# Kernel optimization log

Measured on AMD Instinct MI355X. Metric: run time of the kernel, lower is better.

The kernel has to match this reference:

```python
import jax, jax.numpy as jnp
import numpy as np

B, E, H = 16384, 1024, 16
LN_EPS = 1e-5


def setup_inputs() -> dict:
    key = jax.random.key(0)
    ks = jax.random.split(key, 16)
    s = 0.02  # xavier-ish init scale
    inp = {
        "id_feat": jax.random.normal(ks[0], (B, E), jnp.float32),
        "txt_feat": jax.random.normal(ks[1], (B, E), jnp.float32),
        "vis_feat": jax.random.normal(ks[2], (B, E), jnp.float32),
    }
    i = 3
    for name in ("id", "txt", "vis"):
        inp[f"w_in_{name}"] = jax.random.normal(ks[i], (3 * E, E), jnp.float32) * s; i += 1
        inp[f"b_in_{name}"] = jnp.zeros((3 * E,), jnp.float32)
        inp[f"w_out_{name}"] = jax.random.normal(ks[i], (E, E), jnp.float32) * s; i += 1
        inp[f"b_out_{name}"] = jnp.zeros((E,), jnp.float32)
    inp["w_fuse"] = jax.random.normal(ks[i], (E, 3 * E), jnp.float32) * s
    inp["b_fuse"] = jnp.zeros((E,), jnp.float32)
    inp["ln_g"] = jnp.ones((E,), jnp.float32)
    inp["ln_b"] = jnp.zeros((E,), jnp.float32)
    return inp


def _mha(q, kv, w_in, b_in, w_out, b_out):
    """torch nn.MultiheadAttention (batch_first, eval mode). q: [B,1,E], kv: [B,K,E]."""
    D = E // H
    wq, wk, wv = jnp.split(w_in, 3, axis=0)
    bq, bk, bv = jnp.split(b_in, 3)
    K = kv.shape[1]
    qh = (q @ wq.T + bq).reshape(-1, 1, H, D).transpose(0, 2, 1, 3)   # [B,H,1,D]
    kh = (kv @ wk.T + bk).reshape(-1, K, H, D).transpose(0, 2, 1, 3)  # [B,H,K,D]
    vh = (kv @ wv.T + bv).reshape(-1, K, H, D).transpose(0, 2, 1, 3)
    scores = jnp.einsum('bhqd,bhkd->bhqk', qh, kh) / jnp.sqrt(jnp.float32(D))
    attn = jax.nn.softmax(scores, axis=-1)
    o = jnp.einsum('bhqk,bhkd->bhqd', attn, vh).transpose(0, 2, 1, 3).reshape(-1, E)
    return o @ w_out.T + b_out  # [B,E]


def reference(id_feat, txt_feat, vis_feat,
              w_in_id, b_in_id, w_out_id, b_out_id,
              w_in_txt, b_in_txt, w_out_txt, b_out_txt,
              w_in_vis, b_in_vis, w_out_vis, b_out_vis,
              w_fuse, b_fuse, ln_g, ln_b):
    idq, txtq, visq = id_feat[:, None], txt_feat[:, None], vis_feat[:, None]
    a_id = _mha(idq, jnp.concatenate([txtq, visq], axis=1), w_in_id, b_in_id, w_out_id, b_out_id)
    a_txt = _mha(txtq, jnp.concatenate([idq, visq], axis=1), w_in_txt, b_in_txt, w_out_txt, b_out_txt)
    a_vis = _mha(visq, jnp.concatenate([idq, txtq], axis=1), w_in_vis, b_in_vis, w_out_vis, b_out_vis)
    concat = jnp.concatenate([a_id, a_txt, a_vis], axis=1)  # [B, 3E]
    y = concat @ w_fuse.T + b_fuse
    mu = jnp.mean(y, axis=-1, keepdims=True)
    var = jnp.var(y, axis=-1, keepdims=True)
    return (y - mu) / jnp.sqrt(var + LN_EPS) * ln_g + ln_b
```

## Files before the change

kernel.cpp:

```cpp
#include <hip/hip_runtime.h>
#include <stdint.h>

#define B_ROWS 16384
#define E_DIM 1024
#define H_N 16

typedef unsigned short u16;
typedef __attribute__((ext_vector_type(4))) float f32x4;
typedef __attribute__((ext_vector_type(4))) unsigned short u16x4;
typedef __attribute__((ext_vector_type(8))) short bf16x8;

static __device__ __forceinline__ u16 f2bf(float f) {
  union { float f; unsigned u; } x; x.f = f;
  unsigned r = (x.u + 0x7FFFu + ((x.u >> 16) & 1u)) >> 16;
  return (u16)r;
}
static __device__ __forceinline__ float bf2f(u16 h) {
  union { unsigned u; float f; } x; x.u = ((unsigned)h) << 16;
  return x.f;
}

typedef const __attribute__((address_space(1))) void gvoid;
typedef __attribute__((address_space(3))) void lvoid;
static __device__ __forceinline__ void gload16(const void* g, void* l) {
  __builtin_amdgcn_global_load_lds((gvoid*)g, (lvoid*)l, 16, 0, 0);
}

__global__ __launch_bounds__(256) void cvt_f32_bf16(const float* __restrict__ in,
                                                    u16* __restrict__ out, int n4) {
  int stride = gridDim.x * blockDim.x;
  for (int i = blockIdx.x * blockDim.x + threadIdx.x; i < n4; i += stride) {
    f32x4 v = ((const f32x4*)in)[i];
    u16x4 o;
    o.x = f2bf(v.x); o.y = f2bf(v.y); o.z = f2bf(v.z); o.w = f2bf(v.w);
    ((u16x4*)out)[i] = o;
  }
}

__global__ __launch_bounds__(256) void cvt3_f32_bf16(const float* __restrict__ i0,
                                                     const float* __restrict__ i1,
                                                     const float* __restrict__ i2,
                                                     u16* __restrict__ o0,
                                                     u16* __restrict__ o1,
                                                     u16* __restrict__ o2, int n4) {
  int stride = gridDim.x * blockDim.x;
  for (int i = blockIdx.x * blockDim.x + threadIdx.x; i < n4; i += stride) {
    f32x4 a = ((const f32x4*)i0)[i];
    f32x4 b = ((const f32x4*)i1)[i];
    f32x4 c = ((const f32x4*)i2)[i];
    u16x4 x, y, z;
    x.x = f2bf(a.x); x.y = f2bf(a.y); x.z = f2bf(a.z); x.w = f2bf(a.w);
    y.x = f2bf(b.x); y.y = f2bf(b.y); y.z = f2bf(b.z); y.w = f2bf(b.w);
    z.x = f2bf(c.x); z.y = f2bf(c.y); z.z = f2bf(c.z); z.w = f2bf(c.w);
    ((u16x4*)o0)[i] = x;
    ((u16x4*)o1)[i] = y;
    ((u16x4*)o2)[i] = z;
  }
}

__global__ __launch_bounds__(256) void transpose_to_bf16(const float* __restrict__ in,
                                                         u16* __restrict__ out, int n) {
  __shared__ float t[32][33];
  int bx = blockIdx.x * 32;
  int by = blockIdx.y * 32;
  int tx = threadIdx.x, ty = threadIdx.y;
  for (int r = ty; r < 32; r += 8)
    t[r][tx] = in[(size_t)(by + r) * n + bx + tx];
  __syncthreads();
  for (int r = ty; r < 32; r += 8)
    out[(size_t)(bx + r) * n + by + tx] = f2bf(t[tx][r]);
}

__global__ __launch_bounds__(256) void fold_bias(const float* __restrict__ b0,
                                                 const float* __restrict__ b1,
                                                 const float* __restrict__ b2,
                                                 const float* __restrict__ wfuse,
                                                 const float* __restrict__ bfuse,
                                                 float* __restrict__ cb) {
  int wave = threadIdx.x >> 6, lane = threadIdx.x & 63;
  int j = blockIdx.x * 4 + wave;
  const float* wrow = wfuse + (size_t)j * (3 * E_DIM);
  float s = 0.f;
  for (int i = lane; i < E_DIM; i += 64) s += b0[i] * wrow[i];
  for (int i = lane; i < E_DIM; i += 64) s += b1[i] * wrow[E_DIM + i];
  for (int i = lane; i < E_DIM; i += 64) s += b2[i] * wrow[2 * E_DIM + i];
  for (int off = 32; off; off >>= 1) s += __shfl_xor(s, off);
  if (lane == 0) cb[j] = bfuse[j] + s;
}

__global__ __launch_bounds__(256) void concat_bias(const float* __restrict__ bq,
                                                   const float* __restrict__ bo0,
                                                   const float* __restrict__ bo1,
                                                   float* __restrict__ out) {
  int i = blockIdx.x * 256 + threadIdx.x;
  float v;
  if (i < 1024) v = bq[i];
  else if (i < 3072) v = bo0[i];
  else v = bo1[i - 2048];
  out[i] = v;
}

#define BM 256
#define BN 256
#define BK 64

#define RDA(buf, qm, dst)                                                         \
  do {                                                                            \
    _Pragma("unroll") for (int m = 0; m < 4; m++)                                 \
    _Pragma("unroll") for (int kk = 0; kk < 2; kk++) {                            \
      int rl = (qm)*64 + m * 16 + l16;                                            \
      int col = ((kk * 64 + kq * 16) ^ ((l16 & 7) << 4)) >> 1;                    \
      dst[m][kk] = *(const bf16x8*)&lds[buf][wm * 8192 + rl * 64 + col];          \
    }                                                                             \
  } while (0)

#define RDB(buf, qn, dst)                                                         \
  do {                                                                            \
    _Pragma("unroll") for (int n = 0; n < 2; n++)                                 \
    _Pragma("unroll") for (int kk = 0; kk < 2; kk++) {                            \
      int rt = (qn)*128 + wn * 32 + n * 16 + l16;           \
      int col = ((kk * 64 + kq * 16) ^ ((l16 & 7) << 4)) >> 1;                    \
      dst[n][kk] = *(const bf16x8*)&lds[buf][16384 + (rt >> 7) * 8192 +           \
                                             (rt & 127) * 64 + col];              \
    }                                                                             \
  } while (0)

#define MMAQ(qm, qn, A_, B_)                                                      \
  do {                                                                            \
    __builtin_amdgcn_s_setprio(1);                                                \
    _Pragma("unroll") for (int m = 0; m < 4; m++)                                 \
    _Pragma("unroll") for (int n = 0; n < 2; n++)                                 \
    _Pragma("unroll") for (int kk = 0; kk < 2; kk++)                              \
      acc[(qm)*4 + m][(qn)*2 + n] = __builtin_amdgcn_mfma_f32_16x16x32_bf16(      \
          A_[m][kk], B_[n][kk], acc[(qm)*4 + m][(qn)*2 + n], 0, 0, 0);            \
    __builtin_amdgcn_s_setprio(0);                                                \
  } while (0)

#define BAR() __builtin_amdgcn_s_barrier()
#define SCHED() __builtin_amdgcn_sched_barrier(0)
#define LGKM0() asm volatile("s_waitcnt lgkmcnt(0)" ::: "memory")
#define VMC(n) asm volatile("s_waitcnt vmcnt(" #n ")" ::: "memory")

template <int MODE>
__global__ __launch_bounds__(512, 2) void gemm256(const u16* __restrict__ A,
                                                  const u16* __restrict__ W,
                                                  void* __restrict__ Cp,
                                                  const float* __restrict__ bias,
                                                  int lda, int ldw, int ldc, int K,
                                                  int nbn, int njb,
                                                  long jsA, long jsW, long jsC, long jsB) {
  __shared__ __align__(16) u16 lds[2][32768];

  const int tid = threadIdx.x;
  const int wave = tid >> 6;
  const int lane = tid & 63;
  const int wm = wave >> 2;
  const int wn = wave & 3;
  const int l16 = lane & 15;
  const int kq = lane >> 4;

  const int nwg = gridDim.x;
  int bid = blockIdx.x;
  int xcd = bid & 7, orig = bid >> 3;
  int q8 = nwg >> 3, r8 = nwg & 7;
  int wg = (xcd < r8 ? xcd * (q8 + 1) : r8 * (q8 + 1) + (xcd - r8) * q8) + orig;
  const int j = wg / njb;
  const int rem = wg - j * njb;
  const int bm = rem / nbn;
  const int bn = rem % nbn;

  const u16* Ab = A + j * jsA + (size_t)bm * BM * lda;
  const u16* Wb = W + j * jsW + (size_t)bn * BN * ldw;

  f32x4 acc[8][4];
#pragma unroll
  for (int i = 0; i < 8; i++)
#pragma unroll
    for (int n = 0; n < 4; n++) acc[i][n] = (f32x4){0.f, 0.f, 0.f, 0.f};

  auto stageH = [&](int buf, int which, int k0) {
    const u16* src = (which >= 2) ? Wb : Ab;
    const int ld = (which >= 2) ? ldw : lda;
    const int h = which & 1;
#pragma unroll
    for (int r = 0; r < 2; r++) {
      int slot = r * 512 + tid;
      int row = h * 128 + (slot >> 3);
      int col = ((slot & 7) ^ (row & 7)) * 8;
      gload16(src + (size_t)row * ld + k0 + col, &lds[buf][which * 8192 + slot * 8]);
    }
  };

  const int nt = K / BK;
  stageH(0, 0, 0); stageH(0, 1, 0); stageH(0, 2, 0); stageH(0, 3, 0);
  VMC(2);
  BAR();
  SCHED();

  bf16x8 a[4][2], b0[2][2], b1[2][2];
  int cur = 0;
  for (int t = 0; t < nt; ++t) {
    const bool pf = (t + 1 < nt);
    const int nb = cur ^ 1;
    const int nk = (t + 1) * BK;
    RDA(cur, 0, a);
    RDB(cur, 0, b0);
    if (pf) { stageH(nb, 0, nk); stageH(nb, 1, nk); stageH(nb, 2, nk); }
    BAR();
    LGKM0();
    SCHED();
    MMAQ(0, 0, a, b0);
    if (pf) VMC(6); else VMC(0);
    BAR();
    SCHED();
    RDB(cur, 1, b1);
    if (pf) stageH(nb, 3, nk);
    BAR();
    LGKM0();
    SCHED();
    MMAQ(0, 1, a, b1);
    BAR();
    RDA(cur, 1, a);
    BAR();
    LGKM0();
    SCHED();
    MMAQ(1, 0, a, b0);
    BAR();
    MMAQ(1, 1, a, b1);
    if (pf) VMC(2); else VMC(0);
    BAR();
    SCHED();
    cur ^= 1;
  }

  const int r0 = kq * 4;
#pragma unroll
  for (int mf = 0; mf < 8; mf++) {
#pragma unroll
    for (int nf = 0; nf < 4; nf++) {
      int row = bm * BM + wm * 128 + mf * 16 + r0;
      int col = bn * BN + (nf >> 1) * 128 + wn * 32 + (nf & 1) * 16 + l16;
      if (MODE == 0) {
        u16* C = (u16*)Cp + j * jsC;
        float bv = bias ? bias[j * jsB + col] : 0.f;
#pragma unroll
        for (int r = 0; r < 4; r++)
          C[(size_t)(row + r) * ldc + col] = f2bf(acc[mf][nf][r] + bv);
      } else {
        float* C = (float*)Cp + j * jsC;
        float bv = bias[j * jsB + col];
#pragma unroll
        for (int r = 0; r < 4; r++)
          C[(size_t)(row + r) * ldc + col] = acc[mf][nf][r] + bv;
      }
    }
  }
}

__global__ __launch_bounds__(256) void attn_combine3(const u16* __restrict__ Pb,
                                                     long jsP, u16* __restrict__ Oc) {
  int gw = blockIdx.x * 4 + (threadIdx.x >> 6);
  int lane = threadIdx.x & 63;
  int b = gw >> 4, h = gw & 15;
  int d = h * 64 + lane;
  size_t prow = (size_t)b * 5120;
  const int j1a[3] = {1, 0, 0}, j2a[3] = {2, 2, 1};
  const int offA[3] = {1024, 1024, 3072}, offB[3] = {1024, 3072, 3072};
#pragma unroll
  for (int m = 0; m < 3; m++) {
    const u16* Pq = Pb + m * jsP;
    const u16* Pa = Pb + j1a[m] * jsP;
    const u16* Pc = Pb + j2a[m] * jsP;
    float q = bf2f(Pq[prow + d]);
    float k1 = bf2f(Pa[prow + offA[m] + d]);
    float v1 = bf2f(Pa[prow + offA[m] + 1024 + d]);
    float k2 = bf2f(Pc[prow + offB[m] + d]);
    float v2 = bf2f(Pc[prow + offB[m] + 1024 + d]);
    float s1 = q * k1, s2 = q * k2;
    for (int off = 32; off; off >>= 1) {
      s1 += __shfl_xor(s1, off);
      s2 += __shfl_xor(s2, off);
    }
    s1 *= 0.125f; s2 *= 0.125f;
    float mx = fmaxf(s1, s2);
    float e1 = __expf(s1 - mx), e2 = __expf(s2 - mx);
    float rn = 1.f / (e1 + e2);
    Oc[(size_t)b * 3072 + m * 1024 + d] = f2bf((e1 * rn) * v1 + (e2 * rn) * v2);
  }
}

__global__ __launch_bounds__(256) void layernorm_inplace(float* __restrict__ y,
                                                         const float* __restrict__ g,
                                                         const float* __restrict__ b) {
  int row = blockIdx.x, tid = threadIdx.x;
  float* yr = y + (size_t)row * E_DIM;
  f32x4 v = ((const f32x4*)yr)[tid];
  float s = v.x + v.y + v.z + v.w;
  float sq = v.x * v.x + v.y * v.y + v.z * v.z + v.w * v.w;
  for (int off = 32; off; off >>= 1) {
    s += __shfl_xor(s, off);
    sq += __shfl_xor(sq, off);
  }
  __shared__ float rs[4], rq[4];
  int wave = tid >> 6, lane = tid & 63;
  if (lane == 0) { rs[wave] = s; rq[wave] = sq; }
  __syncthreads();
  s = rs[0] + rs[1] + rs[2] + rs[3];
  sq = rq[0] + rq[1] + rq[2] + rq[3];
  float mu = s * (1.f / E_DIM);
  float var = sq * (1.f / E_DIM) - mu * mu;
  float rstd = rsqrtf(var + 1e-5f);
  f32x4 gg = ((const f32x4*)g)[tid];
  f32x4 bb = ((const f32x4*)b)[tid];
  f32x4 o;
  o.x = (v.x - mu) * rstd * gg.x + bb.x;
  o.y = (v.y - mu) * rstd * gg.y + bb.y;
  o.z = (v.z - mu) * rstd * gg.z + bb.z;
  o.w = (v.w - mu) * rstd * gg.w + bb.w;
  ((f32x4*)yr)[tid] = o;
}

extern "C" void kernel_launch(void* const* d_in, const int* in_sizes, int n_in,
                              void* d_out, int out_size, void* d_ws, size_t ws_size,
                              hipStream_t stream) {
  const float* feat[3] = {(const float*)d_in[0], (const float*)d_in[1], (const float*)d_in[2]};
  const float* w_in[3] = {(const float*)d_in[3], (const float*)d_in[7], (const float*)d_in[11]};
  const float* b_in[3] = {(const float*)d_in[4], (const float*)d_in[8], (const float*)d_in[12]};
  const float* w_out[3] = {(const float*)d_in[5], (const float*)d_in[9], (const float*)d_in[13]};
  const float* b_out[3] = {(const float*)d_in[6], (const float*)d_in[10], (const float*)d_in[14]};
  const float* w_fuse = (const float*)d_in[15];
  const float* b_fuse = (const float*)d_in[16];
  const float* ln_g = (const float*)d_in[17];
  const float* ln_b = (const float*)d_in[18];

  auto A256 = [](size_t b) { return (b + 255) & ~(size_t)255; };
  const size_t EE = (size_t)E_DIM * E_DIM;

  const size_t persist = 3 * A256(5 * EE * 2) + 3 * A256(5 * E_DIM * 4) +
                         A256(3 * EE * 2) + A256(E_DIM * 4);

  int CH = 2048;
  bool bigOcat;
  {
    size_t need = persist + 3 * A256((size_t)CH * E_DIM * 2) +
                  3 * A256((size_t)CH * 5 * E_DIM * 2) +
                  A256((size_t)B_ROWS * 3 * E_DIM * 2);
    bigOcat = (need <= ws_size);
  }
  if (!bigOcat) {
    CH = B_ROWS;
    while (CH > 256) {
      size_t pool = 3 * A256((size_t)CH * E_DIM * 2) + 3 * A256((size_t)CH * 5 * E_DIM * 2) +
                    A256((size_t)CH * 3 * E_DIM * 2);
      if (persist + pool <= ws_size) break;
      CH -= 256;
    }
  }

  char* p = (char*)d_ws;
  auto alloc = [&](size_t bytes) {
    void* r = (void*)p;
    p += A256(bytes);
    return r;
  };

  u16* Wcat[3];
  for (int i = 0; i < 3; i++) Wcat[i] = (u16*)alloc(5 * EE * 2);
  float* bcat[3];
  for (int i = 0; i < 3; i++) bcat[i] = (float*)alloc(5 * E_DIM * 4);
  u16* Mcat = (u16*)alloc(3 * EE * 2);
  float* cb = (float*)alloc(E_DIM * 4);

  char* pool = p;

  const int oth[3][2] = {{1, 2}, {0, 2}, {0, 1}};

  for (int j = 0; j < 3; j++) {
    int o0 = oth[j][0], o1 = oth[j][1];
    cvt_f32_bf16<<<256, 256, 0, stream>>>(w_in[j], Wcat[j], (int)(EE / 4));
    cvt_f32_bf16<<<512, 256, 0, stream>>>(w_in[o0] + EE, Wcat[j] + EE, (int)(2 * EE / 4));
    cvt_f32_bf16<<<512, 256, 0, stream>>>(w_in[o1] + EE, Wcat[j] + 3 * EE, (int)(2 * EE / 4));
    concat_bias<<<5 * E_DIM / 256, 256, 0, stream>>>(b_in[j], b_in[o0], b_in[o1], bcat[j]);
  }

  {
    u16* wfusebf = (u16*)pool;
    u16* woutT = (u16*)(pool + A256(3 * EE * 2));
    cvt_f32_bf16<<<1024, 256, 0, stream>>>(w_fuse, wfusebf, (int)(3 * EE / 4));
    dim3 tb(32, 8);
    for (int f = 0; f < 3; f++) {
      transpose_to_bf16<<<dim3(E_DIM / 32, E_DIM / 32), tb, 0, stream>>>(w_out[f], woutT, E_DIM);
      int ntiles = (E_DIM / BM) * (E_DIM / BN);
      gemm256<0><<<ntiles, 512, 0, stream>>>(
          wfusebf + f * E_DIM, woutT, (void*)(Mcat + f * E_DIM), nullptr,
          3 * E_DIM, E_DIM, 3 * E_DIM, E_DIM, E_DIM / BN, ntiles, 0, 0, 0, 0);
    }
    fold_bias<<<E_DIM / 4, 256, 0, stream>>>(b_out[0], b_out[1], b_out[2], w_fuse, b_fuse, cb);
  }

  {
    char* q = pool;
    auto palloc = [&](size_t bytes) {
      void* r = (void*)q;
      q += A256(bytes);
      return r;
    };
    u16* fb0 = (u16*)palloc(3 * A256((size_t)CH * E_DIM * 2));
    u16* P0 = (u16*)palloc(3 * A256((size_t)CH * 5 * E_DIM * 2));
    u16* Ocat = (u16*)palloc(bigOcat ? (size_t)B_ROWS * 3 * E_DIM * 2
                                     : (size_t)CH * 3 * E_DIM * 2);
    const long jsA = (long)CH * E_DIM;
    const long jsP = (long)CH * 5 * E_DIM;
    const long jsW = (long)(A256(5 * EE * 2) / 2);
    const long jsB = 5 * E_DIM;

    for (int row0 = 0; row0 < B_ROWS; row0 += CH) {
      int rows = B_ROWS - row0 < CH ? B_ROWS - row0 : CH;
      cvt3_f32_bf16<<<1024, 256, 0, stream>>>(
          feat[0] + (size_t)row0 * E_DIM, feat[1] + (size_t)row0 * E_DIM,
          feat[2] + (size_t)row0 * E_DIM, fb0, fb0 + jsA, fb0 + 2 * jsA,
          rows * (E_DIM / 4));
      const int njb = (rows / BM) * (5 * E_DIM / BN);
      gemm256<0><<<3 * njb, 512, 0, stream>>>(
          fb0, Wcat[0], (void*)P0, bcat[0], E_DIM, E_DIM, 5 * E_DIM, E_DIM,
          5 * E_DIM / BN, njb, jsA, jsW, jsP, jsB);
      u16* Oc = bigOcat ? Ocat + (size_t)row0 * 3 * E_DIM : Ocat;
      attn_combine3<<<rows * H_N / 4, 256, 0, stream>>>(P0, jsP, Oc);
      if (!bigOcat) {
        int nt2 = (rows / BM) * (E_DIM / BN);
        gemm256<1><<<nt2, 512, 0, stream>>>(
            Ocat, Mcat, (void*)((float*)d_out + (size_t)row0 * E_DIM), cb,
            3 * E_DIM, 3 * E_DIM, E_DIM, 3 * E_DIM, E_DIM / BN, nt2, 0, 0, 0, 0);
      }
    }
    if (bigOcat) {
      int nt2 = (B_ROWS / BM) * (E_DIM / BN);
      gemm256<1><<<nt2, 512, 0, stream>>>(
          Ocat, Mcat, d_out, cb, 3 * E_DIM, 3 * E_DIM, E_DIM, 3 * E_DIM,
          E_DIM / BN, nt2, 0, 0, 0, 0);
    }
  }

  layernorm_inplace<<<B_ROWS, 256, 0, stream>>>((float*)d_out, ln_g, ln_b);
}
```

Measured before the change: 1.073 ms.

## Process two N-tiles per workgroup in projection GEMM, prefetching across tile boundary

The GEMM kernel gains a tiles-per-block parameter so one workgroup computes several consecutive N-tiles with the same A rows. The K-loop prefetch carries over into the next tile, which hides the prologue load, and each tile's epilogue stores and clears the accumulators. The input-projection GEMM uses two tiles per block, halving its grid and amortising the per-block fill cost. The trade-off is fewer workgroups and a full vmcnt drain after each epilogue, which may lower occupancy and load balance.

```diff
diff --git a/kernel.cpp b/kernel.cpp
--- a/kernel.cpp
+++ b/kernel.cpp
@@ -147,7 +147,7 @@
                                                   void* __restrict__ Cp,
                                                   const float* __restrict__ bias,
                                                   int lda, int ldw, int ldc, int K,
-                                                  int nbn, int njb,
+                                                  int nbn, int njb, int tpb,
                                                   long jsA, long jsW, long jsC, long jsB) {
   __shared__ __align__(16) u16 lds[2][32768];
 
@@ -167,10 +167,10 @@
   const int j = wg / njb;
   const int rem = wg - j * njb;
   const int bm = rem / nbn;
-  const int bn = rem % nbn;
+  const int bn0 = (rem % nbn) * tpb;
 
   const u16* Ab = A + j * jsA + (size_t)bm * BM * lda;
-  const u16* Wb = W + j * jsW + (size_t)bn * BN * ldw;
+  const u16* Wb0 = W + j * jsW + (size_t)bn0 * BN * ldw;
 
   f32x4 acc[8][4];
 #pragma unroll
@@ -178,8 +178,8 @@
 #pragma unroll
     for (int n = 0; n < 4; n++) acc[i][n] = (f32x4){0.f, 0.f, 0.f, 0.f};
 
-  auto stageH = [&](int buf, int which, int k0) {
-    const u16* src = (which >= 2) ? Wb : Ab;
+  auto stageH = [&](int buf, int which, int k0, int ttn) {
+    const u16* src = (which >= 2) ? (Wb0 + (size_t)ttn * BN * ldw) : Ab;
     const int ld = (which >= 2) ? ldw : lda;
     const int h = which & 1;
 #pragma unroll
@@ -192,68 +192,75 @@
   };
 
   const int nt = K / BK;
-  stageH(0, 0, 0); stageH(0, 1, 0); stageH(0, 2, 0); stageH(0, 3, 0);
+  const int r0 = kq * 4;
+
+  stageH(0, 0, 0, 0); stageH(0, 1, 0, 0); stageH(0, 2, 0, 0); stageH(0, 3, 0, 0);
   VMC(2);
   BAR();
   SCHED();
 
   bf16x8 a[4][2], b0[2][2], b1[2][2];
   int cur = 0;
-  for (int t = 0; t < nt; ++t) {
-    const bool pf = (t + 1 < nt);
-    const int nb = cur ^ 1;
-    const int nk = (t + 1) * BK;
-    RDA(cur, 0, a);
-    RDB(cur, 0, b0);
-    if (pf) { stageH(nb, 0, nk); stageH(nb, 1, nk); stageH(nb, 2, nk); }
-    BAR();
-    LGKM0();
-    SCHED();
-    MMAQ(0, 0, a, b0);
-    if (pf) VMC(6); else VMC(0);
-    BAR();
-    SCHED();
-    RDB(cur, 1, b1);
-    if (pf) stageH(nb, 3, nk);
-    BAR();
-    LGKM0();
-    SCHED();
-    MMAQ(0, 1, a, b1);
-    BAR();
-    RDA(cur, 1, a);
-    BAR();
-    LGKM0();
-    SCHED();
-    MMAQ(1, 0, a, b0);
-    BAR();
-    MMAQ(1, 1, a, b1);
-    if (pf) VMC(2); else VMC(0);
-    BAR();
-    SCHED();
-    cur ^= 1;
-  }
-
-  const int r0 = kq * 4;
-#pragma unroll
-  for (int mf = 0; mf < 8; mf++) {
-#pragma unroll
-    for (int nf = 0; nf < 4; nf++) {
-      int row = bm * BM + wm * 128 + mf * 16 + r0;
-      int col = bn * BN + (nf >> 1) * 128 + wn * 32 + (nf & 1) * 16 + l16;
-      if (MODE == 0) {
-        u16* C = (u16*)Cp + j * jsC;
-        float bv = bias ? bias[j * jsB + col] : 0.f;
-#pragma unroll
-        for (int r = 0; r < 4; r++)
-          C[(size_t)(row + r) * ldc + col] = f2bf(acc[mf][nf][r] + bv);
-      } else {
-        float* C = (float*)Cp + j * jsC;
-        float bv = bias[j * jsB + col];
-#pragma unroll
-        for (int r = 0; r < 4; r++)
-          C[(size_t)(row + r) * ldc + col] = acc[mf][nf][r] + bv;
+  for (int tt = 0; tt < tpb; ++tt) {
+    for (int t = 0; t < nt; ++t) {
+      int nt_t = t + 1, ntt = tt;
+      if (nt_t == nt) { nt_t = 0; ntt = tt + 1; }
+      const bool pf = (ntt < tpb);
+      const int nb = cur ^ 1;
+      const int nk = nt_t * BK;
+      RDA(cur, 0, a);
+      RDB(cur, 0, b0);
+      if (pf) { stageH(nb, 0, nk, ntt); stageH(nb, 1, nk, ntt); stageH(nb, 2, nk, ntt); }
+      BAR();
+      LGKM0();
+      SCHED();
+      MMAQ(0, 0, a, b0);
+      if (pf) VMC(6); else VMC(0);
+      BAR();
+      SCHED();
+      RDB(cur, 1, b1);
+      if (pf) stageH(nb, 3, nk, ntt);
+      BAR();
+      LGKM0();
+      SCHED();
+      MMAQ(0, 1, a, b1);
+      BAR();
+      RDA(cur, 1, a);
+      BAR();
+      LGKM0();
+      SCHED();
+      MMAQ(1, 0, a, b0);
+      BAR();
+      MMAQ(1, 1, a, b1);
+      if (pf) VMC(2); else VMC(0);
+      BAR();
+      SCHED();
+      cur ^= 1;
+    }
+    const int bnG = bn0 + tt;
+#pragma unroll
+    for (int mf = 0; mf < 8; mf++) {
+#pragma unroll
+      for (int nf = 0; nf < 4; nf++) {
+        int row = bm * BM + wm * 128 + mf * 16 + r0;
+        int col = bnG * BN + (nf >> 1) * 128 + wn * 32 + (nf & 1) * 16 + l16;
+        if (MODE == 0) {
+          u16* C = (u16*)Cp + j * jsC;
+          float bv = bias ? bias[j * jsB + col] : 0.f;
+#pragma unroll
+          for (int r = 0; r < 4; r++)
+            C[(size_t)(row + r) * ldc + col] = f2bf(acc[mf][nf][r] + bv);
+        } else {
+          float* C = (float*)Cp + j * jsC;
+          float bv = bias[j * jsB + col];
+#pragma unroll
+          for (int r = 0; r < 4; r++)
+            C[(size_t)(row + r) * ldc + col] = acc[mf][nf][r] + bv;
+        }
+        acc[mf][nf] = (f32x4){0.f, 0.f, 0.f, 0.f};
       }
     }
+    if (tt + 1 < tpb) { VMC(0); }
   }
 }
 
@@ -393,7 +400,7 @@
       int ntiles = (E_DIM / BM) * (E_DIM / BN);
       gemm256<0><<<ntiles, 512, 0, stream>>>(
           wfusebf + f * E_DIM, woutT, (void*)(Mcat + f * E_DIM), nullptr,
-          3 * E_DIM, E_DIM, 3 * E_DIM, E_DIM, E_DIM / BN, ntiles, 0, 0, 0, 0);
+          3 * E_DIM, E_DIM, 3 * E_DIM, E_DIM, E_DIM / BN, ntiles, 1, 0, 0, 0, 0);
     }
     fold_bias<<<E_DIM / 4, 256, 0, stream>>>(b_out[0], b_out[1], b_out[2], w_fuse, b_fuse, cb);
   }
@@ -420,24 +427,25 @@
           feat[0] + (size_t)row0 * E_DIM, feat[1] + (size_t)row0 * E_DIM,
           feat[2] + (size_t)row0 * E_DIM, fb0, fb0 + jsA, fb0 + 2 * jsA,
           rows * (E_DIM / 4));
-      const int njb = (rows / BM) * (5 * E_DIM / BN);
+      const int nbnp = (5 * E_DIM / BN) / 2;
+      const int njb = (rows / BM) * nbnp;
       gemm256<0><<<3 * njb, 512, 0, stream>>>(
           fb0, Wcat[0], (void*)P0, bcat[0], E_DIM, E_DIM, 5 * E_DIM, E_DIM,
-          5 * E_DIM / BN, njb, jsA, jsW, jsP, jsB);
+          nbnp, njb, 2, jsA, jsW, jsP, jsB);
       u16* Oc = bigOcat ? Ocat + (size_t)row0 * 3 * E_DIM : Ocat;
       attn_combine3<<<rows * H_N / 4, 256, 0, stream>>>(P0, jsP, Oc);
       if (!bigOcat) {
         int nt2 = (rows / BM) * (E_DIM / BN);
         gemm256<1><<<nt2, 512, 0, stream>>>(
             Ocat, Mcat, (void*)((float*)d_out + (size_t)row0 * E_DIM), cb,
-            3 * E_DIM, 3 * E_DIM, E_DIM, 3 * E_DIM, E_DIM / BN, nt2, 0, 0, 0, 0);
+            3 * E_DIM, 3 * E_DIM, E_DIM, 3 * E_DIM, E_DIM / BN, nt2, 1, 0, 0, 0, 0);
       }
     }
     if (bigOcat) {
       int nt2 = (B_ROWS / BM) * (E_DIM / BN);
       gemm256<1><<<nt2, 512, 0, stream>>>(
           Ocat, Mcat, d_out, cb, 3 * E_DIM, 3 * E_DIM, E_DIM, 3 * E_DIM,
-          E_DIM / BN, nt2, 0, 0, 0, 0);
+          E_DIM / BN, nt2, 1, 0, 0, 0, 0);
     }
   }
 
```

Measured after the change: 1.141 ms. 1.06x slower.

## Restructure GEMM main loop to prefetch fragments and cut barriers

Applied to the files above, without the earlier changes.

Reworks the double-buffered GEMM K-loop so the A/B register fragments for the next tile are read from LDS at the end of the previous iteration, using separate a0/a1 register sets. Global-to-LDS staging of the four quarter-tiles is spread across the MFMA phases, and most per-phase barriers are removed. This aims to overlap LDS reads and global loads with MFMA work and reduce synchronization stalls. In exchange it raises register pressure and depends on the vmcnt waits being correct to avoid LDS races.

```diff
diff --git a/kernel.cpp b/kernel.cpp
--- a/kernel.cpp
+++ b/kernel.cpp
@@ -192,44 +192,51 @@
   };
 
   const int nt = K / BK;
+
   stageH(0, 0, 0); stageH(0, 1, 0); stageH(0, 2, 0); stageH(0, 3, 0);
   VMC(2);
   BAR();
   SCHED();
 
-  bf16x8 a[4][2], b0[2][2], b1[2][2];
+  bf16x8 a0[4][2], a1[4][2], b0[2][2], b1[2][2];
+  RDA(0, 0, a0);
+  RDB(0, 0, b0);
+
   int cur = 0;
   for (int t = 0; t < nt; ++t) {
     const bool pf = (t + 1 < nt);
     const int nb = cur ^ 1;
     const int nk = (t + 1) * BK;
-    RDA(cur, 0, a);
-    RDB(cur, 0, b0);
-    if (pf) { stageH(nb, 0, nk); stageH(nb, 1, nk); stageH(nb, 2, nk); }
-    BAR();
-    LGKM0();
-    SCHED();
-    MMAQ(0, 0, a, b0);
-    if (pf) VMC(6); else VMC(0);
-    BAR();
-    SCHED();
-    RDB(cur, 1, b1);
-    if (pf) stageH(nb, 3, nk);
-    BAR();
-    LGKM0();
-    SCHED();
-    MMAQ(0, 1, a, b1);
-    BAR();
-    RDA(cur, 1, a);
-    BAR();
-    LGKM0();
-    SCHED();
-    MMAQ(1, 0, a, b0);
-    BAR();
-    MMAQ(1, 1, a, b1);
+    if (pf) stageH(nb, 0, nk);
     if (pf) VMC(2); else VMC(0);
     BAR();
     SCHED();
+    LGKM0();
+    SCHED();
+    MMAQ(0, 0, a0, b0);
+    RDB(cur, 1, b1);
+    if (pf) stageH(nb, 1, nk);
+    LGKM0();
+    SCHED();
+    MMAQ(0, 1, a0, b1);
+    RDA(cur, 1, a1);
+    if (pf) stageH(nb, 2, nk);
+    LGKM0();
+    SCHED();
+    MMAQ(1, 0, a1, b0);
+    if (pf) {
+      stageH(nb, 3, nk);
+      VMC(2);
+      BAR();
+      SCHED();
+    }
+    LGKM0();
+    SCHED();
+    MMAQ(1, 1, a1, b1);
+    if (pf) {
+      RDA(nb, 0, a0);
+      RDB(nb, 0, b0);
+    }
     cur ^= 1;
   }
 
```

Result: slower. 1.161 ms (+8.2%).
